# Optimization experiments

Measured on AMD Instinct MI355X. Metric: run time of the kernel, lower is better.

The kernel has to match this reference:

```python
import jax, jax.numpy as jnp
import numpy as np

TEMPERATURE = 0.07
B, D = 8192, 256

def _l2norm(x, axis=-1, eps=1e-12):
    # matches torch F.normalize(p=2): x / max(||x||, eps)
    n = jnp.sqrt(jnp.sum(x * x, axis=axis, keepdims=True))
    return x / jnp.maximum(n, eps)

def setup_inputs() -> dict:
    key = jax.random.key(0)
    k1, k2, k3 = jax.random.split(key, 3)
    return {
        "h_emb": jax.random.normal(k1, (B, D), dtype=jnp.float32),
        "r_emb": jax.random.normal(k2, (B, D), dtype=jnp.float32),
        "t_emb": jax.random.normal(k3, (B, D), dtype=jnp.float32),
    }

def reference(h_emb, r_emb, t_emb):
    # query = normalize(h + r); positives/negatives = normalize(t)
    q = _l2norm(h_emb + r_emb, axis=1)          # [B, D]
    t = _l2norm(t_emb, axis=1)                  # [B, D]
    # Dense in-batch similarity. The original builds logits = [pos, off-diag negs];
    # since the diagonal of sim IS the positive similarity, cross-entropy with
    # label 0 equals logsumexp over the full row minus the diagonal entry.
    sim = jnp.einsum('bd,nd->bn', q, t) / TEMPERATURE   # [B, B]
    pos = jnp.diagonal(sim)                              # [B]
    loss = jnp.mean(jax.nn.logsumexp(sim, axis=1) - pos)
    return loss
```

## Files before the change

### kernel.cpp

```cpp
#include <hip/hip_runtime.h>
#include <hip/hip_bf16.h>

#define B_DIM 8192
#define D_DIM 256
#define GRID_GEMM 512
#define NT 16

constexpr float INV_T = 14.285714285714286f;

typedef __bf16 bf16x8 __attribute__((ext_vector_type(8)));
typedef float  f32x16 __attribute__((ext_vector_type(16)));

__device__ inline unsigned short f2bf(float f) {
    union { float f; unsigned u; } x; x.f = f;
    unsigned r = x.u + 0x7fffu + ((x.u >> 16) & 1u);
    return (unsigned short)(r >> 16);
}

__global__ __launch_bounds__(256) void norm_kernel(
    const float* __restrict__ h, const float* __restrict__ r,
    const float* __restrict__ t,
    unsigned short* __restrict__ qws, unsigned short* __restrict__ tws,
    float* __restrict__ rowsum, float* __restrict__ diagsum, int* __restrict__ ticket)
{
    if (blockIdx.x == 0) {
        float4* rs4 = (float4*)rowsum;
#pragma unroll
        for (int i = 0; i < 8; ++i)
            rs4[threadIdx.x * 8 + i] = make_float4(0.f, 0.f, 0.f, 0.f);
        if (threadIdx.x == 0) { *diagsum = 0.f; *ticket = 0; }
    }

    const int wave = threadIdx.x >> 6;
    const int lane = threadIdx.x & 63;
    const int wg   = blockIdx.x * 4 + wave;

#pragma unroll
    for (int i = 0; i < 2; ++i) {
        const int row = wg * 2 + i;
        float4 a = ((const float4*)h)[row * 64 + lane];
        float4 b = ((const float4*)r)[row * 64 + lane];
        float4 v = make_float4(a.x + b.x, a.y + b.y, a.z + b.z, a.w + b.w);
        float s = v.x * v.x + v.y * v.y + v.z * v.z + v.w * v.w;
#pragma unroll
        for (int off = 32; off; off >>= 1) s += __shfl_xor(s, off, 64);
        float scale = 1.0f / fmaxf(sqrtf(s), 1e-12f);
        ushort4 o;
        o.x = f2bf(v.x * scale); o.y = f2bf(v.y * scale);
        o.z = f2bf(v.z * scale); o.w = f2bf(v.w * scale);
        ((ushort4*)qws)[row * 64 + lane] = o;
    }

    {
        const int ks  = lane >> 2;
        const int hi2 = (lane >> 1) & 1;
        const int sub = lane & 1;
#pragma unroll
        for (int i = 0; i < 2; ++i) {
            const int row = wg * 2 + i;
            float4 v = ((const float4*)t)[row * 64 + lane];
            float s = v.x * v.x + v.y * v.y + v.z * v.z + v.w * v.w;
#pragma unroll
            for (int off = 32; off; off >>= 1) s += __shfl_xor(s, off, 64);
            float scale = 1.0f / fmaxf(sqrtf(s), 1e-12f);
            ushort4 o;
            o.x = f2bf(v.x * scale); o.y = f2bf(v.y * scale);
            o.z = f2bf(v.z * scale); o.w = f2bf(v.w * scale);
            size_t slot16 = ((size_t)((row >> 5) * 16 + ks) * 64
                             + (size_t)(hi2 * 32 + (row & 31)));
            *(ushort4*)((unsigned char*)tws + slot16 * 16 + sub * 8) = o;
        }
    }
}

__global__ __launch_bounds__(256, 2) void gemm_lse_kernel(
    const unsigned char* __restrict__ qws, const unsigned char* __restrict__ tws,
    float* __restrict__ rowsum, float* __restrict__ diagsum,
    int* __restrict__ ticket, float* __restrict__ out)
{
    __shared__ float wred[4];
    __shared__ int lastflag;

    const int tid  = threadIdx.x;
    const int lane = tid & 63;
    const int w    = tid >> 6;
    const int l31  = lane & 31;
    const int hi   = lane >> 5;

    const int cc   = blockIdx.x & 15;
    const int rb   = blockIdx.x >> 4;
    const int row0 = rb * 256 + w * 64;
    const int col0 = cc * 512;
    const int tile0 = cc * 16;

    bf16x8 a[2][16];
    {
        const unsigned char* abase = qws + (size_t)(row0 + l31) * 512 + hi * 16;
#pragma unroll
        for (int rt = 0; rt < 2; ++rt)
#pragma unroll
            for (int ks = 0; ks < 16; ++ks)
                a[rt][ks] = *(const bf16x8*)(abase + rt * (32 * 512) + ks * 32);
    }

    f32x16 rowacc[2] = {};
    float diagacc = 0.f;

    for (int nt = 0; nt < NT; ++nt) {
        const unsigned char* bb = tws + (size_t)(tile0 + nt) * 16384 + lane * 16;

        f32x16 acc0 = {}, acc1 = {};
#pragma unroll
        for (int ks = 0; ks < 16; ++ks) {
            bf16x8 b = *(const bf16x8*)(bb + ks * 1024);
            acc0 = __builtin_amdgcn_mfma_f32_32x32x16_bf16(a[0][ks], b, acc0, 0, 0, 0);
            acc1 = __builtin_amdgcn_mfma_f32_32x32x16_bf16(a[1][ks], b, acc1, 0, 0, 0);
        }

#pragma unroll
        for (int g = 0; g < 16; ++g) {
            rowacc[0][g] += __expf(fmaf(acc0[g], INV_T, -INV_T));
            rowacc[1][g] += __expf(fmaf(acc1[g], INV_T, -INV_T));
        }

        const int c0t = col0 + nt * 32;
        if (c0t == row0) {
#pragma unroll
            for (int g = 0; g < 16; ++g) {
                int rm = (g & 3) + 8 * (g >> 2) + 4 * hi;
                if (l31 == rm) diagacc += acc0[g] * INV_T;
            }
        }
        if (c0t == row0 + 32) {
#pragma unroll
            for (int g = 0; g < 16; ++g) {
                int rm = (g & 3) + 8 * (g >> 2) + 4 * hi;
                if (l31 == rm) diagacc += acc1[g] * INV_T;
            }
        }
    }

#pragma unroll
    for (int rt = 0; rt < 2; ++rt)
#pragma unroll
        for (int g = 0; g < 16; ++g) {
            float s = rowacc[rt][g];
            s += __shfl_xor(s, 1, 64);
            s += __shfl_xor(s, 2, 64);
            s += __shfl_xor(s, 4, 64);
            s += __shfl_xor(s, 8, 64);
            s += __shfl_xor(s, 16, 64);
            if (l31 == 0) {
                int grow = row0 + rt * 32 + (g & 3) + 8 * (g >> 2) + 4 * hi;
                atomicAdd(&rowsum[grow], s);
            }
        }

    float dsum = diagacc;
#pragma unroll
    for (int off = 32; off; off >>= 1) dsum += __shfl_xor(dsum, off, 64);
    if (lane == 0 && dsum != 0.f) atomicAdd(diagsum, dsum);

    __syncthreads();
    if (tid == 0) {
        __threadfence();
        int old = __hip_atomic_fetch_add(ticket, 1, __ATOMIC_ACQ_REL,
                                         __HIP_MEMORY_SCOPE_AGENT);
        lastflag = (old == GRID_GEMM - 1);
    }
    __syncthreads();
    if (!lastflag) return;

    float lsum = 0.f;
    for (int rr = tid; rr < B_DIM; rr += 256) {
        float rs = __hip_atomic_load(&rowsum[rr], __ATOMIC_RELAXED,
                                     __HIP_MEMORY_SCOPE_AGENT);
        lsum += __logf(rs);
    }
#pragma unroll
    for (int off = 32; off; off >>= 1) lsum += __shfl_xor(lsum, off, 64);
    if (lane == 0) wred[w] = lsum;
    __syncthreads();
    if (tid == 0) {
        float ds = __hip_atomic_load(diagsum, __ATOMIC_RELAXED,
                                     __HIP_MEMORY_SCOPE_AGENT);
        float total = wred[0] + wred[1] + wred[2] + wred[3]
                    + (float)B_DIM * INV_T
                    - ds;
        out[0] = total / (float)B_DIM;
    }
}

extern "C" void kernel_launch(void* const* d_in, const int* in_sizes, int n_in,
                              void* d_out, int out_size, void* d_ws, size_t ws_size,
                              hipStream_t stream)
{
    const float* h = (const float*)d_in[0];
    const float* r = (const float*)d_in[1];
    const float* t = (const float*)d_in[2];

    unsigned char* ws = (unsigned char*)d_ws;
    unsigned short* qws = (unsigned short*)ws;
    unsigned short* tws = (unsigned short*)(ws + 4u * 1024 * 1024);
    float* rowsum  = (float*)(ws + 8u * 1024 * 1024);
    float* diagsum = (float*)(ws + 8u * 1024 * 1024 + 32u * 1024);
    int*   ticket  = (int*)  (ws + 8u * 1024 * 1024 + 32u * 1024 + 16);

    norm_kernel<<<1024, 256, 0, stream>>>(h, r, t, qws, tws, rowsum, diagsum, ticket);
    gemm_lse_kernel<<<GRID_GEMM, 256, 0, stream>>>(
        (const unsigned char*)qws, (const unsigned char*)tws,
        rowsum, diagsum, ticket, (float*)d_out);
}
```

Measured before the change: 146.5 us.

## Stage B tiles through LDS with async global_load_lds ring buffer

Each block now prefetches the t-tiles it needs into a 4-slot LDS ring using global_load_lds, two tiles ahead. The four waves read B from LDS instead of each loading it separately from global memory. Q is also written in the same MFMA-swizzled layout as T, so the A-operand loads are coalesced. The change adds 64KB of LDS per block, which may cut occupancy below the launch bound of 2, and it relies on a hand-encoded waitcnt plus a barrier for correctness.

New measurement: 132.4 us. -9.6%, faster.

```diff
diff --git a/kernel.cpp b/kernel.cpp
--- a/kernel.cpp
+++ b/kernel.cpp
@@ -10,6 +10,11 @@
 
 typedef __bf16 bf16x8 __attribute__((ext_vector_type(8)));
 typedef float  f32x16 __attribute__((ext_vector_type(16)));
+
+#define GLOBAL_U32(p) ((const __attribute__((address_space(1))) unsigned int*)(p))
+#define LDS_U32(p)    ((__attribute__((address_space(3))) unsigned int*)(p))
+
+#define WAITCNT_VM8 0x0F78
 
 __device__ inline unsigned short f2bf(float f) {
     union { float f; unsigned u; } x; x.f = f;
@@ -35,29 +40,29 @@
     const int lane = threadIdx.x & 63;
     const int wg   = blockIdx.x * 4 + wave;
 
+    const int ks  = lane >> 2;
+    const int hi2 = (lane >> 1) & 1;
+    const int sub = lane & 1;
+
 #pragma unroll
     for (int i = 0; i < 2; ++i) {
         const int row = wg * 2 + i;
-        float4 a = ((const float4*)h)[row * 64 + lane];
-        float4 b = ((const float4*)r)[row * 64 + lane];
-        float4 v = make_float4(a.x + b.x, a.y + b.y, a.z + b.z, a.w + b.w);
-        float s = v.x * v.x + v.y * v.y + v.z * v.z + v.w * v.w;
-#pragma unroll
-        for (int off = 32; off; off >>= 1) s += __shfl_xor(s, off, 64);
-        float scale = 1.0f / fmaxf(sqrtf(s), 1e-12f);
-        ushort4 o;
-        o.x = f2bf(v.x * scale); o.y = f2bf(v.y * scale);
-        o.z = f2bf(v.z * scale); o.w = f2bf(v.w * scale);
-        ((ushort4*)qws)[row * 64 + lane] = o;
-    }
-
-    {
-        const int ks  = lane >> 2;
-        const int hi2 = (lane >> 1) & 1;
-        const int sub = lane & 1;
-#pragma unroll
-        for (int i = 0; i < 2; ++i) {
-            const int row = wg * 2 + i;
+        {
+            float4 a = ((const float4*)h)[row * 64 + lane];
+            float4 b = ((const float4*)r)[row * 64 + lane];
+            float4 v = make_float4(a.x + b.x, a.y + b.y, a.z + b.z, a.w + b.w);
+            float s = v.x * v.x + v.y * v.y + v.z * v.z + v.w * v.w;
+#pragma unroll
+            for (int off = 32; off; off >>= 1) s += __shfl_xor(s, off, 64);
+            float scale = 1.0f / fmaxf(sqrtf(s), 1e-12f);
+            ushort4 o;
+            o.x = f2bf(v.x * scale); o.y = f2bf(v.y * scale);
+            o.z = f2bf(v.z * scale); o.w = f2bf(v.w * scale);
+            size_t slot16 = ((size_t)((row >> 5) * 16 + ks) * 64
+                             + (size_t)(hi2 * 32 + (row & 31)));
+            *(ushort4*)((unsigned char*)qws + slot16 * 16 + sub * 8) = o;
+        }
+        {
             float4 v = ((const float4*)t)[row * 64 + lane];
             float s = v.x * v.x + v.y * v.y + v.z * v.z + v.w * v.w;
 #pragma unroll
@@ -78,6 +83,7 @@
     float* __restrict__ rowsum, float* __restrict__ diagsum,
     int* __restrict__ ticket, float* __restrict__ out)
 {
+    __shared__ __align__(16) unsigned char ldsB[4][32 * 512];
     __shared__ float wred[4];
     __shared__ int lastflag;
 
@@ -93,26 +99,44 @@
     const int col0 = cc * 512;
     const int tile0 = cc * 16;
 
+#define STAGE(snt, bufi)                                                     \
+    {                                                                        \
+        const unsigned char* gs = tws + (size_t)(tile0 + (snt)) * 16384;     \
+        _Pragma("unroll")                                                    \
+        for (int it = 0; it < 4; ++it)                                       \
+            __builtin_amdgcn_global_load_lds(                                \
+                GLOBAL_U32(gs + (it * 256 + tid) * 16),                      \
+                LDS_U32(&ldsB[bufi][(it * 256 + tid) * 16]), 16, 0, 0);      \
+    }
+
+    STAGE(0, 0);
+    STAGE(1, 1);
+
     bf16x8 a[2][16];
     {
-        const unsigned char* abase = qws + (size_t)(row0 + l31) * 512 + hi * 16;
+        const unsigned char* abase = qws + (size_t)row0 * 512 + lane * 16;
 #pragma unroll
         for (int rt = 0; rt < 2; ++rt)
 #pragma unroll
             for (int ks = 0; ks < 16; ++ks)
-                a[rt][ks] = *(const bf16x8*)(abase + rt * (32 * 512) + ks * 32);
+                a[rt][ks] = *(const bf16x8*)(abase + rt * 16384 + ks * 1024);
     }
 
     f32x16 rowacc[2] = {};
     float diagacc = 0.f;
 
     for (int nt = 0; nt < NT; ++nt) {
-        const unsigned char* bb = tws + (size_t)(tile0 + nt) * 16384 + lane * 16;
-
+        const int snt = (nt + 2 < NT) ? nt + 2 : NT - 1;
+        STAGE(snt, (nt + 2) & 3);
+
+        __builtin_amdgcn_s_waitcnt(WAITCNT_VM8);
+        __builtin_amdgcn_s_barrier();
+
+        const unsigned char* bbuf = ldsB[nt & 3] + lane * 16;
         f32x16 acc0 = {}, acc1 = {};
 #pragma unroll
         for (int ks = 0; ks < 16; ++ks) {
-            bf16x8 b = *(const bf16x8*)(bb + ks * 1024);
+            bf16x8 b = *(const bf16x8*)(bbuf + ks * 1024);
             acc0 = __builtin_amdgcn_mfma_f32_32x32x16_bf16(a[0][ks], b, acc0, 0, 0, 0);
             acc1 = __builtin_amdgcn_mfma_f32_32x32x16_bf16(a[1][ks], b, acc1, 0, 0, 0);
         }
```
